# Optimization experiments

Hardware: AMD Instinct MI355X
Metric: run time of the kernel (lower is better)

Reference implementation:

```python
import jax, jax.numpy as jnp
import numpy as np

D_MODEL = 512
N_HEADS = 8
NEG_INF = -1e9
LN_EPS = 1e-5


def setup_inputs() -> dict:
    key = jax.random.key(0)
    ks = jax.random.split(key, 8)
    B, V, T1, D = 8, 32, 192, D_MODEL
    T = T1 - 1
    x = jax.random.normal(ks[0], (B, V, T1, D), dtype=jnp.float32)
    obs_mask = jax.random.randint(ks[1], (B, V, T), 0, 2, dtype=jnp.int32)
    padding_mask = jax.random.randint(ks[2], (B, T), 0, 2) > 0
    s = 1.0 / np.sqrt(D)
    gamma = jnp.ones((D,), jnp.float32)
    beta = jnp.zeros((D,), jnp.float32)
    W_qkv = jax.random.normal(ks[3], (D, 3 * D), dtype=jnp.float32) * s
    W_proj = jax.random.normal(ks[4], (D, D), dtype=jnp.float32) * s
    b_proj = jnp.zeros((D,), jnp.float32)
    return {"x": x, "obs_mask": obs_mask, "padding_mask": padding_mask,
            "gamma": gamma, "beta": beta, "W_qkv": W_qkv,
            "W_proj": W_proj, "b_proj": b_proj}


def reference(x, obs_mask, padding_mask, gamma, beta, W_qkv, W_proj, b_proj):
    B, V, T1, D = x.shape
    H, dh = N_HEADS, D // N_HEADS
    BV = B * V

    x_flat = x.reshape(BV, T1, D)
    # LayerNorm (eval-mode dropout == identity)
    mu = jnp.mean(x_flat, axis=-1, keepdims=True)
    var = jnp.var(x_flat, axis=-1, keepdims=True)
    x_norm = (x_flat - mu) * jax.lax.rsqrt(var + LN_EPS) * gamma + beta

    qkv = (x_norm @ W_qkv).reshape(BV, T1, 3, H, dh)
    qkv = jnp.transpose(qkv, (2, 0, 3, 1, 4))  # (3, BV, H, T1, dh)
    q, k, v = qkv[0], qkv[1], qkv[2]

    # additive observation bias: mask[i] + mask[j] in {0,1,2}
    obs_ext = jnp.concatenate(
        [jnp.ones((B, V, 1), obs_mask.dtype), obs_mask], axis=2
    ).reshape(BV, T1).astype(jnp.float32)
    attn_bias = obs_ext[:, :, None] + obs_ext[:, None, :]  # (BV, T1, T1)

    # padding mask: True = valid; invalid pairs get -1e9
    pad_ext = jnp.concatenate(
        [jnp.ones((B, 1), bool), padding_mask], axis=1
    )  # (B, T1)
    pad_flat = jnp.broadcast_to(pad_ext[:, None, :], (B, V, T1)).reshape(BV, T1)
    pad_attn = pad_flat[:, :, None] & pad_flat[:, None, :]
    attn_bias = attn_bias + jnp.where(pad_attn, 0.0, NEG_INF)

    scale = 1.0 / jnp.sqrt(jnp.asarray(dh, jnp.float32))
    scores = jnp.einsum("bhqd,bhkd->bhqk", q, k) * scale + attn_bias[:, None]
    attn = jax.nn.softmax(scores, axis=-1)
    out = jnp.einsum("bhqk,bhkd->bhqd", attn, v)  # (BV, H, T1, dh)
    out = jnp.transpose(out, (0, 2, 1, 3)).reshape(BV, T1, D)
    out = out @ W_proj + b_proj
    return (x_flat + out).reshape(B, V, T1, D)
```

## Files before the change

kernel.cpp:

```cpp
#include <hip/hip_runtime.h>

#define DEVI __device__ __forceinline__

typedef __attribute__((ext_vector_type(8))) short short8;
typedef __attribute__((ext_vector_type(4))) float f32x4;

DEVI unsigned short f2bf(float f) {
  unsigned int u = __float_as_uint(f);
  u += 0x7fffu + ((u >> 16) & 1u);
  return (unsigned short)(u >> 16);
}

DEVI void gload16(const void* g, void* l) {
  __builtin_amdgcn_global_load_lds((__attribute__((address_space(1))) void*)g,
                                   (__attribute__((address_space(3))) void*)l, 16, 0, 0);
}

__global__ __launch_bounds__(256) void ln_kernel(
    const float* __restrict__ x, const float* __restrict__ gamma,
    const float* __restrict__ beta, unsigned short* __restrict__ xn,
    const float* __restrict__ Wq, const float* __restrict__ Wp,
    unsigned short* __restrict__ Wtq, unsigned short* __restrict__ Wtp) {
  int tid = threadIdx.x;
  if (blockIdx.x >= 12288) {
    int idx = (blockIdx.x - 12288) * 256 + tid;
    const int stride = 512 * 256;
    for (int i = idx; i < 1536 * 512; i += stride) {
      int n = i >> 9, k = i & 511;
      Wtq[i] = f2bf(Wq[(size_t)k * 1536 + n]);
    }
    for (int i = idx; i < 512 * 512; i += stride) {
      int n = i >> 9, k = i & 511;
      Wtp[i] = f2bf(Wp[(size_t)k * 512 + n]);
    }
    return;
  }
  int w = tid >> 6, l = tid & 63;
  size_t row = (size_t)blockIdx.x * 4 + w;
  const float* xr = x + row * 512 + l * 8;
  float4 v0 = *(const float4*)xr;
  float4 v1 = *(const float4*)(xr + 4);
  float s  = v0.x + v0.y + v0.z + v0.w + v1.x + v1.y + v1.z + v1.w;
  float ss = v0.x*v0.x + v0.y*v0.y + v0.z*v0.z + v0.w*v0.w
           + v1.x*v1.x + v1.y*v1.y + v1.z*v1.z + v1.w*v1.w;
  #pragma unroll
  for (int m = 1; m < 64; m <<= 1) {
    s  += __shfl_xor(s,  m);
    ss += __shfl_xor(ss, m);
  }
  float mean = s * (1.f / 512.f);
  float var  = ss * (1.f / 512.f) - mean * mean;
  float rstd = rsqrtf(var + 1e-5f);
  float4 g0 = *(const float4*)(gamma + l * 8);
  float4 g1 = *(const float4*)(gamma + l * 8 + 4);
  float4 b0 = *(const float4*)(beta + l * 8);
  float4 b1 = *(const float4*)(beta + l * 8 + 4);
  short8 ov;
  ov[0] = (short)f2bf((v0.x - mean) * rstd * g0.x + b0.x);
  ov[1] = (short)f2bf((v0.y - mean) * rstd * g0.y + b0.y);
  ov[2] = (short)f2bf((v0.z - mean) * rstd * g0.z + b0.z);
  ov[3] = (short)f2bf((v0.w - mean) * rstd * g0.w + b0.w);
  ov[4] = (short)f2bf((v1.x - mean) * rstd * g1.x + b1.x);
  ov[5] = (short)f2bf((v1.y - mean) * rstd * g1.y + b1.y);
  ov[6] = (short)f2bf((v1.z - mean) * rstd * g1.z + b1.z);
  ov[7] = (short)f2bf((v1.w - mean) * rstd * g1.w + b1.w);
  *(short8*)(xn + row * 512 + l * 8) = ov;
}

template<int EPI>
__global__ __launch_bounds__(256, 2) void gemm_bt(
    const unsigned short* __restrict__ A, const unsigned short* __restrict__ Bt,
    unsigned short* __restrict__ Cbf, float* __restrict__ Cf,
    const float* __restrict__ bias, const float* __restrict__ resid,
    int M, int N, int K, int nbx) {
  __shared__ __align__(16) char gsmem[32768];
  unsigned short* As = (unsigned short*)gsmem;
  unsigned short* Bs = As + 128 * 64;
  float* Cs = (float*)gsmem;
  int tid = threadIdx.x;
  int w = tid >> 6, l = tid & 63;
  int nwg = nbx * gridDim.y;
  int lin = blockIdx.y * nbx + blockIdx.x;
  int cpx = nwg >> 3;
  int swz = (lin & 7) * cpx + (lin >> 3);
  int bn = swz % nbx, bm = swz / nbx;
  int wr = w >> 1, wc = w & 1;
  int t8 = tid >> 3;
  int c8s = (((tid & 7) ^ ((tid >> 3) & 7)) * 8);
  int lr = l & 15, lk4 = l >> 4;
  const unsigned short* Ab = A + (size_t)bm * 128 * K;
  const unsigned short* Bb = Bt + (size_t)bn * 128 * K;
  f32x4 zero = {0.f, 0.f, 0.f, 0.f};
  f32x4 acc[4][4];
  #pragma unroll
  for (int i = 0; i < 4; i++)
    #pragma unroll
    for (int j = 0; j < 4; j++) acc[i][j] = zero;

  for (int k0 = 0; k0 < K; k0 += 64) {
    #pragma unroll
    for (int i = 0; i < 4; i++) {
      gload16(Ab + (size_t)(i * 32 + t8) * K + k0 + c8s, (char*)As + i * 4096 + w * 1024);
      gload16(Bb + (size_t)(i * 32 + t8) * K + k0 + c8s, (char*)Bs + i * 4096 + w * 1024);
    }
    __syncthreads();
    #pragma unroll
    for (int kk = 0; kk < 2; kk++) {
      short8 a[4], b[4];
      #pragma unroll
      for (int i = 0; i < 4; i++) {
        int ra = wr * 64 + i * 16 + lr;
        a[i] = *(const short8*)((const char*)As + ra * 128 +
                                (((kk * 64 + lk4 * 16)) ^ ((ra & 7) << 4)));
      }
      #pragma unroll
      for (int j = 0; j < 4; j++) {
        int rb = wc * 64 + j * 16 + lr;
        b[j] = *(const short8*)((const char*)Bs + rb * 128 +
                                (((kk * 64 + lk4 * 16)) ^ ((rb & 7) << 4)));
      }
      #pragma unroll
      for (int i = 0; i < 4; i++)
        #pragma unroll
        for (int j = 0; j < 4; j++)
          acc[i][j] = __builtin_amdgcn_mfma_f32_16x16x32_bf16(a[i], b[j], acc[i][j], 0, 0, 0);
    }
    __syncthreads();
  }
  if (EPI == 0) {
    int rb = bm * 128 + wr * 64 + lk4 * 4;
    int cb = bn * 128 + wc * 64 + lr;
    #pragma unroll
    for (int i = 0; i < 4; i++)
      #pragma unroll
      for (int j = 0; j < 4; j++)
        #pragma unroll
        for (int r = 0; r < 4; r++)
          Cbf[(size_t)(rb + i * 16 + r) * N + (cb + j * 16)] = f2bf(acc[i][j][r]);
  } else {
    #pragma unroll
    for (int c = 0; c < 2; c++) {
      if (wr == c) {
        #pragma unroll
        for (int i = 0; i < 4; i++)
          #pragma unroll
          for (int j = 0; j < 4; j++)
            #pragma unroll
            for (int r = 0; r < 4; r++)
              Cs[(i * 16 + lk4 * 4 + r) * 128 + wc * 64 + j * 16 + lr] = acc[i][j][r];
      }
      __syncthreads();
      #pragma unroll
      for (int it = 0; it < 8; it++) {
        int lrow = it * 8 + (tid >> 5);
        int col = (tid & 31) * 4;
        float4 v = *(const float4*)&Cs[lrow * 128 + col];
        int grow = bm * 128 + c * 64 + lrow;
        int gcol = bn * 128 + col;
        float4 bi = *(const float4*)(bias + gcol);
        float4 rs = *(const float4*)(resid + (size_t)grow * N + gcol);
        v.x += bi.x + rs.x;
        v.y += bi.y + rs.y;
        v.z += bi.z + rs.z;
        v.w += bi.w + rs.w;
        *(float4*)(Cf + (size_t)grow * N + gcol) = v;
      }
      __syncthreads();
    }
  }
}

__global__ __launch_bounds__(256, 2) void attn_kernel(
    const unsigned short* __restrict__ qkv, unsigned short* __restrict__ aout,
    const int* __restrict__ obs_mask, const int* __restrict__ pad_mask) {
  __shared__ __align__(16) char smem[52480];
  char* KsB = smem;
  unsigned short* Vt = (unsigned short*)smem;
  char* Pw = smem + 25600;
  float* obsb = (float*)(smem + 50176);
  int*   padb = (int*)(smem + 50944);
  float* kbT  = (float*)(smem + 51712);

  const float LOG2E = 1.44269504f;
  const float K2 = 0.18033688f;
  const float C2 = -1.44269504e9f;

  int h = blockIdx.x, bv = blockIdx.y;
  int tid = threadIdx.x, w = tid >> 6, l = tid & 63;
  int lr = l & 15, lk4 = l >> 4;
  int b = bv >> 5;
  for (int t = tid; t < 192; t += 256) {
    float obs = (t == 0) ? 1.f : (float)obs_mask[bv * 191 + (t - 1)];
    int pad = (t == 0) ? 1 : pad_mask[b * 191 + (t - 1)];
    obsb[t] = obs;
    padb[t] = pad;
    kbT[t] = obs * LOG2E + (pad ? 0.f : C2);
  }
  const unsigned short* base = qkv + (size_t)bv * 192 * 1536 + h * 64;

  #pragma unroll
  for (int it = 0; it < 6; it++) {
    int s = it * 256 + tid;
    int row = s >> 3, slot = s & 7;
    gload16(base + (size_t)row * 1536 + 512 + (slot ^ (row & 7)) * 8,
            KsB + it * 4096 + w * 1024);
  }
  short8 qf[3][2];
  #pragma unroll
  for (int i = 0; i < 3; i++)
    #pragma unroll
    for (int kk = 0; kk < 2; kk++)
      qf[i][kk] = *(const short8*)(base + (size_t)(w * 48 + i * 16 + lr) * 1536 + kk * 32 + lk4 * 8);

  __syncthreads();
  f32x4 zero = {0.f, 0.f, 0.f, 0.f};
  f32x4 sc[3][12];
  #pragma unroll
  for (int i = 0; i < 3; i++)
    #pragma unroll
    for (int j = 0; j < 12; j++) sc[i][j] = zero;
  #pragma unroll
  for (int kk = 0; kk < 2; kk++) {
    short8 bb[12];
    #pragma unroll
    for (int j = 0; j < 12; j++) {
      int row = j * 16 + lr;
      bb[j] = *(const short8*)(KsB + row * 128 + ((kk * 64 + lk4 * 16) ^ ((row & 7) << 4)));
    }
    __builtin_amdgcn_s_setprio(1);
    #pragma unroll
    for (int i = 0; i < 3; i++)
      #pragma unroll
      for (int j = 0; j < 12; j++)
        sc[i][j] = __builtin_amdgcn_mfma_f32_16x16x32_bf16(qf[i][kk], bb[j], sc[i][j], 0, 0, 0);
    __builtin_amdgcn_s_setprio(0);
  }
  __syncthreads();

  #pragma unroll
  for (int it = 0; it < 3; it++) {
    int s = it * 256 + tid;
    int kp = s >> 3;
    int d0 = (s & 7) * 8;
    short8 va = *(const short8*)(base + (size_t)(kp * 2) * 1536 + 1024 + d0);
    short8 vb = *(const short8*)(base + (size_t)(kp * 2 + 1) * 1536 + 1024 + d0);
    int slot = ((d0 >> 3) & 7) << 4;
    #pragma unroll
    for (int e = 0; e < 8; e++) {
      int byte = (((d0 + e) * 400 + kp * 4) ^ slot);
      *(unsigned int*)((char*)Vt + byte) =
          ((unsigned int)(unsigned short)vb[e] << 16) | (unsigned int)(unsigned short)va[e];
    }
  }

  float cT[12];
  #pragma unroll
  for (int j = 0; j < 12; j++) cT[j] = kbT[j * 16 + lr];
  unsigned int pf[3][2][12];
  #pragma unroll
  for (int i = 0; i < 3; i++) {
    #pragma unroll
    for (int r = 0; r < 4; r++) {
      int row = w * 48 + i * 16 + lk4 * 4 + r;
      float ro2 = obsb[row] * LOG2E;
      int rp = padb[row];
      float sum = 0.f;
      #pragma unroll
      for (int j = 0; j < 12; j++) {
        float vv = fmaf(sc[i][j][r], K2, ro2 + cT[j]);
        float e = rp ? __builtin_amdgcn_exp2f(vv) : 1.0f;
        sc[i][j][r] = e;
        sum += e;
      }
      #pragma unroll
      for (int m = 1; m < 16; m <<= 1) sum += __shfl_xor(sum, m);
      float inv = 1.f / sum;
      #pragma unroll
      for (int j = 0; j < 12; j++) sc[i][j][r] *= inv;
    }
    #pragma unroll
    for (int j = 0; j < 12; j++) {
      asm("v_cvt_pk_bf16_f32 %0, %1, %2"
          : "=v"(pf[i][0][j]) : "v"(sc[i][j][0]), "v"(sc[i][j][1]));
      asm("v_cvt_pk_bf16_f32 %0, %1, %2"
          : "=v"(pf[i][1][j]) : "v"(sc[i][j][2]), "v"(sc[i][j][3]));
    }
  }
  __syncthreads();

  char* Pme = Pw + w * 6144;
  f32x4 o[3][4];
  #pragma unroll
  for (int i = 0; i < 3; i++)
    #pragma unroll
    for (int jd = 0; jd < 4; jd++) o[i][jd] = zero;
  #pragma unroll
  for (int kc = 0; kc < 3; kc++) {
    #pragma unroll
    for (int i = 0; i < 3; i++)
      #pragma unroll
      for (int rp = 0; rp < 2; rp++) {
        int row0 = i * 16 + lk4 * 4 + rp * 2;
        int row1 = row0 + 1;
        #pragma unroll
        for (int jj = 0; jj < 4; jj++) {
          unsigned int v = pf[i][rp][kc * 4 + jj];
          int c2 = (jj * 16 + lr) * 2;
          *(unsigned short*)(Pme + row0 * 128 + (c2 ^ ((row0 & 7) << 4))) = (unsigned short)v;
          *(unsigned short*)(Pme + row1 * 128 + (c2 ^ ((row1 & 7) << 4))) = (unsigned short)(v >> 16);
        }
      }
    asm volatile("s_waitcnt lgkmcnt(0)" ::: "memory");
    __builtin_amdgcn_sched_barrier(0);
    #pragma unroll
    for (int kk = 0; kk < 2; kk++) {
      short8 a[3], bb[4];
      #pragma unroll
      for (int i = 0; i < 3; i++) {
        int ra = i * 16 + lr;
        a[i] = *(const short8*)(Pme + ra * 128 + (((kk * 32 + lk4 * 8) * 2) ^ ((ra & 7) << 4)));
      }
      #pragma unroll
      for (int jd = 0; jd < 4; jd++) {
        int d = jd * 16 + lr;
        int byte = ((d * 400 + (kc * 64 + kk * 32 + lk4 * 8) * 2) ^ (((d >> 3) & 7) << 4));
        bb[jd] = *(const short8*)((const char*)Vt + byte);
      }
      __builtin_amdgcn_s_setprio(1);
      #pragma unroll
      for (int i = 0; i < 3; i++)
        #pragma unroll
        for (int jd = 0; jd < 4; jd++)
          o[i][jd] = __builtin_amdgcn_mfma_f32_16x16x32_bf16(a[i], bb[jd], o[i][jd], 0, 0, 0);
      __builtin_amdgcn_s_setprio(0);
    }
  }

  asm volatile("s_waitcnt lgkmcnt(0)" ::: "memory");
  __builtin_amdgcn_sched_barrier(0);
  #pragma unroll
  for (int i = 0; i < 3; i++)
    #pragma unroll
    for (int jd = 0; jd < 4; jd++)
      #pragma unroll
      for (int h2 = 0; h2 < 2; h2++) {
        unsigned int u;
        asm("v_cvt_pk_bf16_f32 %0, %1, %2"
            : "=v"(u) : "v"(o[i][jd][h2 * 2]), "v"(o[i][jd][h2 * 2 + 1]));
        int row0 = i * 16 + lk4 * 4 + h2 * 2;
        int row1 = row0 + 1;
        int c2 = (jd * 16 + lr) * 2;
        *(unsigned short*)(Pme + row0 * 128 + (c2 ^ ((row0 & 7) << 4))) = (unsigned short)u;
        *(unsigned short*)(Pme + row1 * 128 + (c2 ^ ((row1 & 7) << 4))) = (unsigned short)(u >> 16);
      }
  asm volatile("s_waitcnt lgkmcnt(0)" ::: "memory");
  __builtin_amdgcn_sched_barrier(0);
  unsigned short* ob2 = aout + (size_t)(bv * 192 + w * 48) * 512 + h * 64;
  #pragma unroll
  for (int p = 0; p < 6; p++) {
    int row = p * 8 + (l >> 3);
    int c = l & 7;
    int slot = (row & 7) << 4;
    short8 v = *(const short8*)(Pme + row * 128 + ((c * 16) ^ slot));
    *(short8*)(ob2 + (size_t)row * 512 + c * 8) = v;
  }
}

extern "C" void kernel_launch(void* const* d_in, const int* in_sizes, int n_in,
                              void* d_out, int out_size, void* d_ws, size_t ws_size,
                              hipStream_t stream) {
  const float* x     = (const float*)d_in[0];
  const int*   obs   = (const int*)d_in[1];
  const int*   pad   = (const int*)d_in[2];
  const float* gamma = (const float*)d_in[3];
  const float* beta  = (const float*)d_in[4];
  const float* Wq    = (const float*)d_in[5];
  const float* Wp    = (const float*)d_in[6];
  const float* bp    = (const float*)d_in[7];
  float* out = (float*)d_out;
  char* ws = (char*)d_ws;

  const size_t M = 49152;
  unsigned short* xn  = (unsigned short*)ws;
  unsigned short* qkv = (unsigned short*)(ws + M * 512 * 2);
  unsigned short* Wtq = (unsigned short*)(ws + M * 512 * 2 + M * 1536 * 2);
  unsigned short* Wtp = Wtq + 1536 * 512;

  ln_kernel<<<dim3(12800), dim3(256), 0, stream>>>(x, gamma, beta, xn, Wq, Wp, Wtq, Wtp);
  gemm_bt<0><<<dim3(12, 384), dim3(256), 0, stream>>>(
      xn, Wtq, qkv, nullptr, nullptr, nullptr, 49152, 1536, 512, 12);
  attn_kernel<<<dim3(8, 256), dim3(256), 0, stream>>>(qkv, xn, obs, pad);
  gemm_bt<1><<<dim3(4, 384), dim3(256), 0, stream>>>(
      xn, Wtp, nullptr, out, bp, x, 49152, 512, 512, 4);
}
```

Before: 228.8 us.

## Replace QKV GEMM with 256x256-tile double-buffered direct-to-LDS kernel

Adds a new GEMM kernel for the QKV projection that uses 256x256 output tiles with 512 threads (8 waves, each computing 128x64), double-buffered LDS staging via global_load_lds with XOR swizzling, and explicit vmcnt waits to overlap the next K-tile load with MFMA work. The larger tile raises arithmetic intensity and cuts redundant global reads of A and B compared with the previous 128-row tile. The cost is 128KB of LDS and one block per CU, which limits latency hiding. The epilogue also writes scattered 2-byte stores directly rather than staging through LDS, which may waste write bandwidth.

```diff
diff --git a/kernel.cpp b/kernel.cpp
--- a/kernel.cpp
+++ b/kernel.cpp
@@ -65,6 +65,90 @@
   ov[6] = (short)f2bf((v1.z - mean) * rstd * g1.z + b1.z);
   ov[7] = (short)f2bf((v1.w - mean) * rstd * g1.w + b1.w);
   *(short8*)(xn + row * 512 + l * 8) = ov;
+}
+
+__global__ __launch_bounds__(512, 1) void gemm256(
+    const unsigned short* __restrict__ A, const unsigned short* __restrict__ Bt,
+    unsigned short* __restrict__ Cbf, int M, int N, int K, int nbx) {
+  __shared__ __align__(16) char smem[131072];
+  int tid = threadIdx.x;
+  int wid = tid >> 6, l = tid & 63;
+  int lr = l & 15, g = l >> 4;
+  int wr = wid >> 2, wc = wid & 3;
+  int nwg = nbx * gridDim.y;
+  int lin = blockIdx.y * nbx + blockIdx.x;
+  int cpx = nwg >> 3;
+  int swz = (lin & 7) * cpx + (lin >> 3);
+  int bn = swz % nbx, bm = swz / nbx;
+  const unsigned short* Ab = A + (size_t)bm * 256 * K;
+  const unsigned short* Bb = Bt + (size_t)bn * 256 * K;
+  int t8 = tid >> 3;
+  int c8s = (((tid & 7) ^ (t8 & 7)) * 8);
+
+  f32x4 zero = {0.f, 0.f, 0.f, 0.f};
+  f32x4 acc[8][4];
+  #pragma unroll
+  for (int mi = 0; mi < 8; mi++)
+    #pragma unroll
+    for (int nj = 0; nj < 4; nj++) acc[mi][nj] = zero;
+
+  #pragma unroll
+  for (int c = 0; c < 4; c++) {
+    gload16(Ab + (size_t)(c * 64 + t8) * K + c8s, smem + c * 8192 + wid * 1024);
+    gload16(Bb + (size_t)(c * 64 + t8) * K + c8s, smem + 32768 + c * 8192 + wid * 1024);
+  }
+
+  for (int t = 0; t < 8; ++t) {
+    if (t < 7) {
+      char* dst = smem + ((t + 1) & 1) * 65536;
+      int k0 = (t + 1) * 64;
+      #pragma unroll
+      for (int c = 0; c < 4; c++) {
+        gload16(Ab + (size_t)(c * 64 + t8) * K + k0 + c8s, dst + c * 8192 + wid * 1024);
+        gload16(Bb + (size_t)(c * 64 + t8) * K + k0 + c8s, dst + 32768 + c * 8192 + wid * 1024);
+      }
+      asm volatile("s_waitcnt vmcnt(8)" ::: "memory");
+    } else {
+      asm volatile("s_waitcnt vmcnt(0)" ::: "memory");
+    }
+    __builtin_amdgcn_s_barrier();
+    __builtin_amdgcn_sched_barrier(0);
+    const char* Al = smem + (t & 1) * 65536;
+    const char* Bl = Al + 32768;
+    #pragma unroll
+    for (int ks = 0; ks < 2; ks++) {
+      short8 a[8], b[4];
+      #pragma unroll
+      for (int mi = 0; mi < 8; mi++) {
+        int ra = wr * 128 + mi * 16 + lr;
+        a[mi] = *(const short8*)(Al + ra * 128 + ((ks * 64 + g * 16) ^ ((ra & 7) << 4)));
+      }
+      #pragma unroll
+      for (int nj = 0; nj < 4; nj++) {
+        int rb = wc * 64 + nj * 16 + lr;
+        b[nj] = *(const short8*)(Bl + rb * 128 + ((ks * 64 + g * 16) ^ ((rb & 7) << 4)));
+      }
+      __builtin_amdgcn_s_setprio(1);
+      #pragma unroll
+      for (int mi = 0; mi < 8; mi++)
+        #pragma unroll
+        for (int nj = 0; nj < 4; nj++)
+          acc[mi][nj] = __builtin_amdgcn_mfma_f32_16x16x32_bf16(a[mi], b[nj], acc[mi][nj], 0, 0, 0);
+      __builtin_amdgcn_s_setprio(0);
+    }
+    __builtin_amdgcn_sched_barrier(0);
+    __builtin_amdgcn_s_barrier();
+  }
+
+  int rb0 = bm * 256 + wr * 128 + g * 4;
+  int cb0 = bn * 256 + wc * 64 + lr;
+  #pragma unroll
+  for (int mi = 0; mi < 8; mi++)
+    #pragma unroll
+    for (int nj = 0; nj < 4; nj++)
+      #pragma unroll
+      for (int r = 0; r < 4; r++)
+        Cbf[(size_t)(rb0 + mi * 16 + r) * N + cb0 + nj * 16] = f2bf(acc[mi][nj][r]);
 }
 
 template<int EPI>
@@ -387,8 +471,7 @@
   unsigned short* Wtp = Wtq + 1536 * 512;
 
   ln_kernel<<<dim3(12800), dim3(256), 0, stream>>>(x, gamma, beta, xn, Wq, Wp, Wtq, Wtp);
-  gemm_bt<0><<<dim3(12, 384), dim3(256), 0, stream>>>(
-      xn, Wtq, qkv, nullptr, nullptr, nullptr, 49152, 1536, 512, 12);
+  gemm256<<<dim3(6, 192), dim3(512), 0, stream>>>(xn, Wtq, qkv, 49152, 1536, 512, 6);
   attn_kernel<<<dim3(8, 256), dim3(256), 0, stream>>>(qkv, xn, obs, pad);
   gemm_bt<1><<<dim3(4, 384), dim3(256), 0, stream>>>(
       xn, Wtp, nullptr, out, bp, x, 49152, 512, 512, 4);
```

After: 240.6 us. +5.2%, slower.
